# Optimization experiments

Measured on AMD Instinct MI355X. Metric: run time of the kernel, lower is better.

## Reference

```python
import jax, jax.numpy as jnp
import numpy as np

B, T, C, H = 2, 1024, 1024, 16
D = C // H                      # head_dim = 64
NG, BS = 64, 16                 # HBS groups / block_size (1024 = 64*16)
SQ = 32                         # sqrt_dim (1024 = 32*32)


def layer_norm(x, g, b, eps=1e-5):
    m = jnp.mean(x, axis=-1, keepdims=True)
    v = jnp.var(x, axis=-1, keepdims=True)
    return (x - m) * jax.lax.rsqrt(v + eps) * g + b


def hbs_proj(x, pre_g, pre_b, block_w, w_row, w_col, alpha, bias):
    # HierarchicalBlockShuffleLayer forward (dim=1024, no padding needed)
    xn = layer_norm(x, pre_g, pre_b)
    x_flat = xn.reshape(-1, C)
    # block mixing: per-group 16x16 matmul, then flip feature axis
    g = x_flat.reshape(-1, NG, BS)
    y_mixed = jnp.einsum('ngi,gij->ngj', g, block_w).reshape(-1, C)
    block_out = y_mixed[..., ::-1]
    # monarch branch: 32x32 grid, right-multiply W_col then W_row^T
    grid = x_flat.reshape(-1, SQ, SQ)
    z = jnp.einsum('nij,jc->nic', grid, w_col)
    z = jnp.einsum('nic,rc->nir', z, w_row).reshape(-1, C)
    out = block_out + alpha * z + bias
    return out.reshape(x.shape)


def setup_inputs() -> dict:
    key = jax.random.key(0)
    ks = jax.random.split(key, 12)
    inp = {
        'x': jax.random.normal(ks[0], (B, T, C), jnp.float32),
        'c_attn_w': jax.random.normal(ks[1], (3 * C, C), jnp.float32) * (1.0 / np.sqrt(C)),
        'c_attn_b': jnp.zeros((3 * C,), jnp.float32),
        'focus_gate': jnp.float32(0.0),
        'attn_norm_g': jnp.ones((D,), jnp.float32),
        'attn_norm_b': jnp.zeros((D,), jnp.float32),
        'out_norm_g': jnp.ones((C,), jnp.float32),
        'out_norm_b': jnp.zeros((C,), jnp.float32),
        'proj_pre_g': jnp.ones((C,), jnp.float32),
        'proj_pre_b': jnp.zeros((C,), jnp.float32),
        'proj_block_w': jax.random.normal(ks[2], (NG, BS, BS), jnp.float32) * 0.5 / np.sqrt(BS),
        'proj_w_row': jax.random.normal(ks[3], (SQ, SQ), jnp.float32) * 0.1 / np.sqrt(SQ),
        'proj_w_col': jax.random.normal(ks[4], (SQ, SQ), jnp.float32) * 0.1 / np.sqrt(SQ),
        'proj_alpha': jnp.float32(0.0),
        'proj_bias': jnp.zeros((C,), jnp.float32),
    }
    return inp


def reference(x, c_attn_w, c_attn_b, focus_gate, attn_norm_g, attn_norm_b,
              out_norm_g, out_norm_b, proj_pre_g, proj_pre_b, proj_block_w,
              proj_w_row, proj_w_col, proj_alpha, proj_bias):
    scale = 1.0 / np.sqrt(D)
    qkv = x @ c_attn_w.T + c_attn_b                      # [B,T,3C]
    q, k, v = jnp.split(qkv, 3, axis=2)
    # [B,H,T,D]
    q = q.reshape(B, T, H, D).transpose(0, 2, 1, 3)
    k = k.reshape(B, T, H, D).transpose(0, 2, 1, 3)
    v = v.reshape(B, T, H, D).transpose(0, 2, 1, 3)

    # --- causal linear attention branch (fp32) ---
    Qp = jax.nn.elu(q * scale) + 1.0
    Kp = jax.nn.elu(k * scale) + 1.0
    KV = jnp.einsum('bhtd,bhte->bhtde', Kp, v)           # [B,H,T,D,D]
    KV_cum = jnp.cumsum(KV, axis=2)
    K_cum = jnp.cumsum(Kp, axis=2)
    numer = jnp.einsum('bhtd,bhtde->bhte', Qp, KV_cum)
    denom = jnp.einsum('bhtd,bhtd->bht', Qp, K_cum)[..., None]
    y_lin = numer / (denom + 1e-4)                       # [B,H,T,D]
    y_lin = layer_norm(y_lin.transpose(0, 2, 1, 3), attn_norm_g, attn_norm_b)
    y_lin = y_lin.transpose(0, 2, 1, 3)

    # --- standard causal SDPA branch ---
    scores = jnp.einsum('bhqd,bhkd->bhqk', q, k) * scale
    causal = jnp.tril(jnp.ones((T, T), bool))
    scores = jnp.where(causal, scores, -jnp.inf)
    attn = jax.nn.softmax(scores, axis=-1)
    y_sharp = jnp.einsum('bhqk,bhkd->bhqd', attn, v)

    # --- gated combine + output projection ---
    alpha = jax.nn.sigmoid(focus_gate)
    y = alpha * y_sharp + (1.0 - alpha) * y_lin
    y = y.transpose(0, 2, 1, 3).reshape(B, T, C)
    y = layer_norm(y, out_norm_g, out_norm_b)
    return hbs_proj(y, proj_pre_g, proj_pre_b, proj_block_w,
                    proj_w_row, proj_w_col, proj_alpha, proj_bias)
```

## Files before the change

kernel.cpp:

```cpp
#include <hip/hip_runtime.h>
#include <math.h>

constexpr int T_ = 1024;
constexpr int C_ = 1024;
constexpr int H_ = 16;
constexpr int D_ = 64;
#define SCALE 0.125f

typedef unsigned short u16;
typedef __attribute__((ext_vector_type(8))) short short8;
typedef __attribute__((ext_vector_type(4))) float f32x4;

__device__ __forceinline__ float elu1(float x) { return x > 0.f ? x + 1.f : expf(x); }

__device__ __forceinline__ u16 f2bf(float f) {
    union { float f; unsigned u; } c; c.f = f;
    unsigned r = (c.u + 0x7fffu + ((c.u >> 16) & 1u)) >> 16;
    return (u16)r;
}
__device__ __forceinline__ float bf2f(u16 u) {
    union { unsigned u; float f; } c; c.u = (unsigned)u << 16;
    return c.f;
}

#define GLL16(g, l)                                                            \
    __builtin_amdgcn_global_load_lds(                                          \
        (const __attribute__((address_space(1))) void*)(g),                    \
        (__attribute__((address_space(3))) void*)(l), 16, 0, 0)

__global__ __launch_bounds__(256) void k0_cast(
    const float* __restrict__ s, u16* __restrict__ d, int n4)
{
    int i = blockIdx.x * 256 + threadIdx.x;
    if (i < n4) {
        float4 v = reinterpret_cast<const float4*>(s)[i];
        ushort4 o;
        o.x = f2bf(v.x); o.y = f2bf(v.y); o.z = f2bf(v.z); o.w = f2bf(v.w);
        reinterpret_cast<ushort4*>(d)[i] = o;
    }
}

__global__ __launch_bounds__(256) void k1_qkv(
    const u16* __restrict__ xbf, const u16* __restrict__ wbf,
    const float* __restrict__ bias,
    u16* __restrict__ qb, u16* __restrict__ kb, u16* __restrict__ vb)
{
    __shared__ __align__(16) u16 As[128 * 32];
    __shared__ __align__(16) u16 Bs[128 * 32];
    const int tid = threadIdx.x;
    const int wave = tid >> 6, lane = tid & 63;
    const int quad = lane >> 4, l15 = lane & 15;
    const int m0 = blockIdx.y << 7, n0 = blockIdx.x << 7;
    const int wm = (wave >> 1) << 6, wn = (wave & 1) << 6;

    const int rowS = (wave << 5) + (lane >> 2);
    const int seg8 = (lane & 3) << 3;
    const u16* gA1 = xbf + (size_t)(m0 + rowS) * 1024 + seg8;
    const u16* gA2 = gA1 + (size_t)16 * 1024;
    const u16* gB1 = wbf + (size_t)(n0 + rowS) * 1024 + seg8;
    const u16* gB2 = gB1 + (size_t)16 * 1024;
    u16* lA1 = &As[(wave << 5) * 32];
    u16* lA2 = lA1 + 16 * 32;
    u16* lB1 = &Bs[(wave << 5) * 32];
    u16* lB2 = lB1 + 16 * 32;

    f32x4 zero4 = {0.f, 0.f, 0.f, 0.f};
    f32x4 acc[4][4];
#pragma unroll
    for (int i = 0; i < 4; i++)
#pragma unroll
        for (int j = 0; j < 4; j++) acc[i][j] = zero4;

    for (int k0 = 0; k0 < 1024; k0 += 32) {
        GLL16(gA1 + k0, lA1);
        GLL16(gA2 + k0, lA2);
        GLL16(gB1 + k0, lB1);
        GLL16(gB2 + k0, lB2);
        __syncthreads();
        short8 a[4], b[4];
#pragma unroll
        for (int mi = 0; mi < 4; mi++)
            a[mi] = *(const short8*)&As[(wm + mi * 16 + l15) * 32 + (quad << 3)];
#pragma unroll
        for (int ni = 0; ni < 4; ni++)
            b[ni] = *(const short8*)&Bs[(wn + ni * 16 + l15) * 32 + (quad << 3)];
#pragma unroll
        for (int mi = 0; mi < 4; mi++)
#pragma unroll
            for (int ni = 0; ni < 4; ni++)
                acc[mi][ni] = __builtin_amdgcn_mfma_f32_16x16x32_bf16(
                    a[mi], b[ni], acc[mi][ni], 0, 0, 0);
        __syncthreads();
    }
#pragma unroll
    for (int ni = 0; ni < 4; ni++) {
        int n_g = n0 + wn + ni * 16 + l15;
        int which = n_g >> 10;
        int h = (n_g >> 6) & 15;
        int d = n_g & 63;
        u16* dst = (which == 0) ? qb : (which == 1) ? kb : vb;
        float bz = bias[n_g];
#pragma unroll
        for (int mi = 0; mi < 4; mi++) {
#pragma unroll
            for (int reg = 0; reg < 4; reg++) {
                int m = m0 + wm + mi * 16 + (quad << 2) + reg;
                int bi = m >> 10, t = m & 1023;
                dst[((size_t)(bi * 16 + h) << 16) + ((size_t)t << 6) + d] =
                    f2bf(acc[mi][ni][reg] + bz);
            }
        }
    }
}

__global__ __launch_bounds__(256) void k_vt(
    const u16* __restrict__ vb, u16* __restrict__ vtb)
{
    const int t0 = blockIdx.x << 6, bh = blockIdx.y;
    __shared__ __align__(16) u16 Vs[64][72];
    const int tid = threadIdx.x;
#pragma unroll
    for (int u = 0; u < 2; u++) {
        int idx = (tid + (u << 8)) << 3;
        int r = idx >> 6, c = idx & 63;
        *(uint4*)&Vs[r][c] =
            *(const uint4*)&vb[((size_t)bh << 16) + ((size_t)(t0 + r) << 6) + c];
    }
    __syncthreads();
#pragma unroll
    for (int u = 0; u < 2; u++) {
        int idx = (tid + (u << 8)) << 3;
        int dd = idx >> 6, c0 = idx & 63;
        union { u16 s[8]; uint4 v; } tmp;
#pragma unroll
        for (int j = 0; j < 8; j++) tmp.s[j] = Vs[c0 + j][dd];
        *(uint4*)&vtb[((size_t)((bh << 6) + dd) << 10) + t0 + c0] = tmp.v;
    }
}

__global__ __launch_bounds__(256) void k2a_chunkkv(
    const u16* __restrict__ kb, const u16* __restrict__ vb,
    float* __restrict__ Sg, float* __restrict__ svg)
{
    const int chunk = blockIdx.x, bh = blockIdx.y;
    const int t0 = chunk << 6;
    __shared__ float Ks[64][65];
    __shared__ float Vs[64][65];
    const int tid = threadIdx.x;
    const u16* kp = kb + (size_t)bh * T_ * D_;
    const u16* vp = vb + (size_t)bh * T_ * D_;
#pragma unroll
    for (int ii = 0; ii < 16; ii++) {
        int idx = tid + (ii << 8);
        int row = idx >> 6, col = idx & 63;
        Ks[row][col] = elu1(bf2f(kp[(size_t)(t0 + row) * D_ + col]) * SCALE);
        Vs[row][col] = bf2f(vp[(size_t)(t0 + row) * D_ + col]);
    }
    __syncthreads();
    const int tr = tid >> 4, tc = tid & 15;
    const int d0 = tr * 4, e0 = tc * 4;
    float acc[4][4] = {};
    for (int c = 0; c < 64; c++) {
        float a[4], b[4];
#pragma unroll
        for (int i = 0; i < 4; i++) a[i] = Ks[c][d0 + i];
#pragma unroll
        for (int j = 0; j < 4; j++) b[j] = Vs[c][e0 + j];
#pragma unroll
        for (int i = 0; i < 4; i++)
#pragma unroll
            for (int j = 0; j < 4; j++) acc[i][j] += a[i] * b[j];
    }
    float* so = Sg + ((size_t)bh * 16 + chunk) * 4096;
#pragma unroll
    for (int i = 0; i < 4; i++) {
        float4 o = {acc[i][0], acc[i][1], acc[i][2], acc[i][3]};
        *reinterpret_cast<float4*>(&so[(d0 + i) * 64 + e0]) = o;
    }
    if (tc == 0) {
#pragma unroll
        for (int i = 0; i < 4; i++) {
            float s = 0.f;
            for (int c = 0; c < 64; c++) s += Ks[c][d0 + i];
            svg[((size_t)bh * 16 + chunk) * 64 + d0 + i] = s;
        }
    }
}

__global__ __launch_bounds__(256) void k2s_scan(
    float* __restrict__ Sg, float* __restrict__ svg)
{
    int gid = blockIdx.x * 256 + threadIdx.x;
    if (gid < 131072) {
        int bh = gid >> 12, e = gid & 4095;
        float* base = Sg + ((size_t)bh << 16) + e;
        float v[16];
#pragma unroll
        for (int c = 0; c < 16; c++) v[c] = base[(size_t)c << 12];
        float run = 0.f;
#pragma unroll
        for (int c = 0; c < 16; c++) {
            base[(size_t)c << 12] = run;
            run += v[c];
        }
    } else if (gid < 131072 + 2048) {
        int g2 = gid - 131072;
        int bh = g2 >> 6, d = g2 & 63;
        float* base = svg + ((size_t)bh << 10) + d;
        float v[16];
#pragma unroll
        for (int c = 0; c < 16; c++) v[c] = base[c << 6];
        float run = 0.f;
#pragma unroll
        for (int c = 0; c < 16; c++) {
            base[c << 6] = run;
            run += v[c];
        }
    }
}

__global__ __launch_bounds__(256) void k2b_lin(
    const u16* __restrict__ qbp, const u16* __restrict__ kbp,
    const u16* __restrict__ vbp,
    const float* __restrict__ Sg, const float* __restrict__ svg,
    const float* __restrict__ ang, const float* __restrict__ anb,
    float* __restrict__ ylin)
{
    const int chunk = blockIdx.x, bh = blockIdx.y;
    const int t0 = chunk << 6;
    __shared__ __align__(16) float bufA[64][68];
    __shared__ float bufQ[64][65];
    __shared__ float bufK[64][65];
    __shared__ float svec[64];
    const int tid = threadIdx.x;
    const u16* qp = qbp + (size_t)bh * T_ * D_;
    const u16* kp = kbp + (size_t)bh * T_ * D_;
    const u16* vp = vbp + (size_t)bh * T_ * D_;
    const float* sp = Sg + (((size_t)bh * 16 + chunk) << 12);
#pragma unroll
    for (int u = 0; u < 4; u++) {
        int idx = (tid + (u << 8)) << 2;
        int dd = idx >> 6, e = idx & 63;
        *(float4*)&bufA[dd][e] = *(const float4*)&sp[idx];
    }
    if (tid < 64) svec[tid] = svg[(((size_t)bh * 16 + chunk) << 6) + tid];
#pragma unroll
    for (int ii = 0; ii < 16; ii++) {
        int idx = tid + (ii << 8);
        int row = idx >> 6, col = idx & 63;
        bufQ[col][row] = elu1(bf2f(qp[(size_t)(t0 + row) * D_ + col]) * SCALE);
    }
    __syncthreads();
    const int tr = tid >> 4, tc = tid & 15;
    const int r0 = tr * 4, c0 = tc * 4;
    float N[4][4] = {};
    float pden[4];
    for (int dd = 0; dd < 64; dd++) {
        float a[4], b[4];
#pragma unroll
        for (int i = 0; i < 4; i++) a[i] = bufQ[dd][r0 + i];
#pragma unroll
        for (int j = 0; j < 4; j++) b[j] = bufA[dd][c0 + j];
#pragma unroll
        for (int i = 0; i < 4; i++)
#pragma unroll
            for (int j = 0; j < 4; j++) N[i][j] += a[i] * b[j];
    }
#pragma unroll
    for (int i = 0; i < 4; i++) {
        float s = 0.f;
#pragma unroll
        for (int j = 0; j < 4; j++) s += bufQ[c0 + j][r0 + i] * svec[c0 + j];
        pden[i] = s;
    }
    __syncthreads();
#pragma unroll
    for (int ii = 0; ii < 16; ii++) {
        int idx = tid + (ii << 8);
        int row = idx >> 6, col = idx & 63;
        bufK[col][row] = elu1(bf2f(kp[(size_t)(t0 + row) * D_ + col]) * SCALE);
        bufA[row][col] = bf2f(vp[(size_t)(t0 + row) * D_ + col]);
    }
    __syncthreads();
    float sc[4][4] = {};
    for (int dd = 0; dd < 64; dd++) {
        float a[4], b[4];
#pragma unroll
        for (int i = 0; i < 4; i++) a[i] = bufQ[dd][r0 + i];
#pragma unroll
        for (int j = 0; j < 4; j++) b[j] = bufK[dd][c0 + j];
#pragma unroll
        for (int i = 0; i < 4; i++)
#pragma unroll
            for (int j = 0; j < 4; j++) sc[i][j] += a[i] * b[j];
    }
    __syncthreads();
#pragma unroll
    for (int i = 0; i < 4; i++) {
        float s = 0.f;
#pragma unroll
        for (int j = 0; j < 4; j++) {
            float pv = ((c0 + j) <= (r0 + i)) ? sc[i][j] : 0.f;
            bufQ[c0 + j][r0 + i] = pv;
            s += pv;
        }
        pden[i] += s;
    }
#pragma unroll
    for (int i = 0; i < 4; i++) {
#pragma unroll
        for (int off = 1; off < 16; off <<= 1)
            pden[i] += __shfl_xor(pden[i], off);
    }
    __syncthreads();
    for (int c = 0; c < 64; c++) {
        float a[4], b[4];
#pragma unroll
        for (int i = 0; i < 4; i++) a[i] = bufQ[c][r0 + i];
#pragma unroll
        for (int j = 0; j < 4; j++) b[j] = bufA[c][c0 + j];
#pragma unroll
        for (int i = 0; i < 4; i++)
#pragma unroll
            for (int j = 0; j < 4; j++) N[i][j] += a[i] * b[j];
    }
    float yv[4][4], s1[4], s2[4];
#pragma unroll
    for (int i = 0; i < 4; i++) {
        float inv = 1.f / (pden[i] + 1e-4f);
        s1[i] = 0.f; s2[i] = 0.f;
#pragma unroll
        for (int j = 0; j < 4; j++) {
            float t = N[i][j] * inv;
            yv[i][j] = t; s1[i] += t; s2[i] += t * t;
        }
    }
#pragma unroll
    for (int i = 0; i < 4; i++) {
#pragma unroll
        for (int off = 1; off < 16; off <<= 1) {
            s1[i] += __shfl_xor(s1[i], off);
            s2[i] += __shfl_xor(s2[i], off);
        }
    }
#pragma unroll
    for (int i = 0; i < 4; i++) {
        float mean = s1[i] * (1.f / 64.f);
        float var = s2[i] * (1.f / 64.f) - mean * mean;
        float rstd = rsqrtf(var + 1e-5f);
        float4 o;
        o.x = (yv[i][0] - mean) * rstd * ang[c0 + 0] + anb[c0 + 0];
        o.y = (yv[i][1] - mean) * rstd * ang[c0 + 1] + anb[c0 + 1];
        o.z = (yv[i][2] - mean) * rstd * ang[c0 + 2] + anb[c0 + 2];
        o.w = (yv[i][3] - mean) * rstd * ang[c0 + 3] + anb[c0 + 3];
        *reinterpret_cast<float4*>(
            &ylin[((size_t)bh * T_ + t0 + r0 + i) * D_ + c0]) = o;
    }
}

__global__ __launch_bounds__(256) void k3_sharp(
    const u16* __restrict__ qbp, const u16* __restrict__ kbp,
    const u16* __restrict__ vtb,
    const float* __restrict__ ylin, const float* __restrict__ fg,
    float* __restrict__ ycomb)
{
    const int bh = blockIdx.y;
    __shared__ __align__(16) u16 Qs[64][72];
    __shared__ __align__(16) u16 Ks[64][72];
    __shared__ __align__(16) u16 Vt[64][72];
    __shared__ __align__(16) u16 Pa[64][72];
    const int tid = threadIdx.x;
    const int wave = tid >> 6, lane = tid & 63;
    const int quad = lane >> 4, l15 = lane & 15;
    const float al = 1.f / (1.f + expf(-fg[0]));
    const int bi = bh >> 4, h = bh & 15;
    const f32x4 zero4 = {0.f, 0.f, 0.f, 0.f};

    for (int phase = 0; phase < 2; phase++) {
        const int qi = phase == 0 ? (int)blockIdx.x : 15 - (int)blockIdx.x;
        __syncthreads();
#pragma unroll
        for (int u = 0; u < 2; u++) {
            int idx = (tid + (u << 8)) << 3;
            int r = idx >> 6, c = idx & 63;
            *(uint4*)&Qs[r][c] = *(const uint4*)
                &qbp[((size_t)bh << 16) + ((size_t)((qi << 6) + r) << 6) + c];
        }
        __syncthreads();
        short8 bq[2];
        bq[0] = *(const short8*)&Qs[(wave << 4) + l15][(quad << 3)];
        bq[1] = *(const short8*)&Qs[(wave << 4) + l15][32 + (quad << 3)];
        f32x4 O[4];
#pragma unroll
        for (int dt = 0; dt < 4; dt++) O[dt] = zero4;
        float m_run = -INFINITY, l_run = 0.f;
        const int r_g = (qi << 6) + (wave << 4) + l15;

        for (int ki = 0; ki <= qi; ki++) {
            __syncthreads();
#pragma unroll
            for (int u = 0; u < 2; u++) {
                int idx = (tid + (u << 8)) << 3;
                int r = idx >> 6, c = idx & 63;
                *(uint4*)&Ks[r][c] = *(const uint4*)
                    &kbp[((size_t)bh << 16) + ((size_t)((ki << 6) + r) << 6) + c];
                *(uint4*)&Vt[r][c] = *(const uint4*)
                    &vtb[((size_t)((bh << 6) + r) << 10) + (ki << 6) + c];
            }
            __syncthreads();
            f32x4 st[4];
#pragma unroll
            for (int ct = 0; ct < 4; ct++) st[ct] = zero4;
#pragma unroll
            for (int ks = 0; ks < 2; ks++) {
#pragma unroll
                for (int ct = 0; ct < 4; ct++) {
                    short8 a = *(const short8*)
                        &Ks[(ct << 4) + l15][(ks << 5) + (quad << 3)];
                    st[ct] = __builtin_amdgcn_mfma_f32_16x16x32_bf16(
                        a, bq[ks], st[ct], 0, 0, 0);
                }
            }
            float mloc = -INFINITY;
#pragma unroll
            for (int ct = 0; ct < 4; ct++)
#pragma unroll
                for (int reg = 0; reg < 4; reg++) {
                    int c_g = (ki << 6) + (ct << 4) + (quad << 2) + reg;
                    float s = st[ct][reg] * SCALE;
                    if (c_g > r_g) s = -INFINITY;
                    st[ct][reg] = s;
                    mloc = fmaxf(mloc, s);
                }
            mloc = fmaxf(mloc, __shfl_xor(mloc, 16));
            mloc = fmaxf(mloc, __shfl_xor(mloc, 32));
            float mnew = fmaxf(m_run, mloc);
            float corr = __expf(m_run - mnew);
            m_run = mnew;
            float rsum = 0.f;
#pragma unroll
            for (int ct = 0; ct < 4; ct++) {
                u16 pk[4];
#pragma unroll
                for (int reg = 0; reg < 4; reg++) {
                    float pv = __expf(st[ct][reg] - mnew);
                    rsum += pv;
                    pk[reg] = f2bf(pv);
                }
                unsigned lo = (unsigned)pk[0] | ((unsigned)pk[1] << 16);
                unsigned hi = (unsigned)pk[2] | ((unsigned)pk[3] << 16);
                uint2 pkv; pkv.x = lo; pkv.y = hi;
                *(uint2*)&Pa[(wave << 4) + l15][(ct << 4) + (quad << 2)] = pkv;
            }
            rsum += __shfl_xor(rsum, 16);
            rsum += __shfl_xor(rsum, 32);
            l_run = l_run * corr + rsum;
            float co[4];
#pragma unroll
            for (int reg = 0; reg < 4; reg++)
                co[reg] = __shfl(corr, ((lane >> 4) << 2) + reg);
#pragma unroll
            for (int dt = 0; dt < 4; dt++)
#pragma unroll
                for (int reg = 0; reg < 4; reg++) O[dt][reg] *= co[reg];
#pragma unroll
            for (int ks = 0; ks < 2; ks++) {
                short8 ap = *(const short8*)
                    &Pa[(wave << 4) + l15][(ks << 5) + (quad << 3)];
#pragma unroll
                for (int dt = 0; dt < 4; dt++) {
                    short8 bv = *(const short8*)
                        &Vt[(dt << 4) + l15][(ks << 5) + (quad << 3)];
                    O[dt] = __builtin_amdgcn_mfma_f32_16x16x32_bf16(
                        ap, bv, O[dt], 0, 0, 0);
                }
            }
        }
        float lo4[4];
#pragma unroll
        for (int reg = 0; reg < 4; reg++)
            lo4[reg] = __shfl(l_run, ((lane >> 4) << 2) + reg);
#pragma unroll
        for (int reg = 0; reg < 4; reg++) {
            int t = (qi << 6) + (wave << 4) + (quad << 2) + reg;
            float inv = al / lo4[reg];
#pragma unroll
            for (int dt = 0; dt < 4; dt++) {
                int d = (dt << 4) + l15;
                float yl = ylin[(((size_t)bh << 10) + t) * 64 + d];
                ycomb[((size_t)((bi << 10) + t) << 10) + (h << 6) + d] =
                    O[dt][reg] * inv + (1.f - al) * yl;
            }
        }
    }
}

__global__ __launch_bounds__(256) void k4m(
    const float* __restrict__ wcol, const float* __restrict__ wrow,
    const float* __restrict__ palpha, float* __restrict__ Mg)
{
    const int tid = threadIdx.x;
    const int j = tid >> 3, r0 = (tid & 7) << 2;
    const float al = palpha[0];
    float acc[4] = {0.f, 0.f, 0.f, 0.f};
    for (int c = 0; c < 32; c++) {
        float wc = wcol[(j << 5) + c];
#pragma unroll
        for (int q = 0; q < 4; q++) acc[q] += wc * wrow[((r0 + q) << 5) + c];
    }
    float4 o = {al * acc[0], al * acc[1], al * acc[2], al * acc[3]};
    *reinterpret_cast<float4*>(&Mg[(j << 5) + r0]) = o;
}

__global__ __launch_bounds__(256) void k4_proj(
    const float* __restrict__ ycomb,
    const float* __restrict__ og, const float* __restrict__ ob,
    const float* __restrict__ pg, const float* __restrict__ pb,
    const float* __restrict__ bw, const float* __restrict__ Mg,
    const float* __restrict__ pbias, float* __restrict__ out)
{
    const int tok = blockIdx.x;
    __shared__ float xb[1024];
    __shared__ float red[8];
    const int tid = threadIdx.x;
    const int c0 = tid << 2;
    const float* yrow = ycomb + ((size_t)tok << 10);
    float4 v4 = *reinterpret_cast<const float4*>(yrow + c0);
    float v[4] = {v4.x, v4.y, v4.z, v4.w};
    float s1 = v[0] + v[1] + v[2] + v[3];
    float s2 = v[0]*v[0] + v[1]*v[1] + v[2]*v[2] + v[3]*v[3];
#pragma unroll
    for (int off = 1; off < 64; off <<= 1) {
        s1 += __shfl_xor(s1, off); s2 += __shfl_xor(s2, off);
    }
    if ((tid & 63) == 0) { red[(tid >> 6) * 2] = s1; red[(tid >> 6) * 2 + 1] = s2; }
    __syncthreads();
    s1 = red[0] + red[2] + red[4] + red[6];
    s2 = red[1] + red[3] + red[5] + red[7];
    __syncthreads();
    {
        float mean = s1 * (1.f / 1024.f);
        float var = s2 * (1.f / 1024.f) - mean * mean;
        float rstd = rsqrtf(var + 1e-5f);
#pragma unroll
        for (int q = 0; q < 4; q++)
            v[q] = (v[q] - mean) * rstd * og[c0 + q] + ob[c0 + q];
    }
    s1 = v[0] + v[1] + v[2] + v[3];
    s2 = v[0]*v[0] + v[1]*v[1] + v[2]*v[2] + v[3]*v[3];
#pragma unroll
    for (int off = 1; off < 64; off <<= 1) {
        s1 += __shfl_xor(s1, off); s2 += __shfl_xor(s2, off);
    }
    if ((tid & 63) == 0) { red[(tid >> 6) * 2] = s1; red[(tid >> 6) * 2 + 1] = s2; }
    __syncthreads();
    s1 = red[0] + red[2] + red[4] + red[6];
    s2 = red[1] + red[3] + red[5] + red[7];
    {
        float mean = s1 * (1.f / 1024.f);
        float var = s2 * (1.f / 1024.f) - mean * mean;
        float rstd = rsqrtf(var + 1e-5f);
#pragma unroll
        for (int q = 0; q < 4; q++)
            xb[c0 + q] = (v[q] - mean) * rstd * pg[c0 + q] + pb[c0 + q];
    }
    __syncthreads();
    const int g = tid >> 2;
    const int jb = (tid & 3) << 2;
    float acc[4] = {0.f, 0.f, 0.f, 0.f};
    {
        const float* xg = &xb[g << 4];
        const float* bwg = &bw[(g << 8) + jb];
        for (int i = 0; i < 16; i++) {
            float xv = xg[i];
            float4 wv = *reinterpret_cast<const float4*>(&bwg[i << 4]);
            acc[0] += xv * wv.x; acc[1] += xv * wv.y;
            acc[2] += xv * wv.z; acc[3] += xv * wv.w;
        }
    }
    const int C0 = ((63 - g) << 4) + 12 - jb;
    const int i2 = C0 >> 5, r0 = C0 & 31;
    float z2[4] = {0.f, 0.f, 0.f, 0.f};
    {
        const float* xg = &xb[i2 << 5];
        const float* mg = &Mg[r0];
        for (int j = 0; j < 32; j++) {
            float xv = xg[j];
            float4 mv = *reinterpret_cast<const float4*>(&mg[j << 5]);
            z2[0] += xv * mv.x; z2[1] += xv * mv.y;
            z2[2] += xv * mv.z; z2[3] += xv * mv.w;
        }
    }
    float4 bz = *reinterpret_cast<const float4*>(&pbias[C0]);
    float4 o;
    o.x = acc[3] + z2[0] + bz.x;
    o.y = acc[2] + z2[1] + bz.y;
    o.z = acc[1] + z2[2] + bz.z;
    o.w = acc[0] + z2[3] + bz.w;
    *reinterpret_cast<float4*>(&out[((size_t)tok << 10) + C0]) = o;
}

extern "C" void kernel_launch(void* const* d_in, const int* in_sizes, int n_in,
                              void* d_out, int out_size, void* d_ws, size_t ws_size,
                              hipStream_t stream) {
    const float* x   = (const float*)d_in[0];
    const float* w   = (const float*)d_in[1];
    const float* wb  = (const float*)d_in[2];
    const float* fg  = (const float*)d_in[3];
    const float* ang = (const float*)d_in[4];
    const float* anb = (const float*)d_in[5];
    const float* ong = (const float*)d_in[6];
    const float* onb = (const float*)d_in[7];
    const float* ppg = (const float*)d_in[8];
    const float* ppb = (const float*)d_in[9];
    const float* pbw = (const float*)d_in[10];
    const float* pwr = (const float*)d_in[11];
    const float* pwc = (const float*)d_in[12];
    const float* pal = (const float*)d_in[13];
    const float* pbi = (const float*)d_in[14];

    uint8_t* p = (uint8_t*)d_ws;
    u16* xbf = (u16*)p;  p += (size_t)2048 * 1024 * 2;
    u16* wbf = (u16*)p;  p += (size_t)3072 * 1024 * 2;
    u16* qb  = (u16*)p;  p += (size_t)32 * 1024 * 64 * 2;
    u16* kb  = (u16*)p;  p += (size_t)32 * 1024 * 64 * 2;
    u16* vb  = (u16*)p;  p += (size_t)32 * 1024 * 64 * 2;
    u16* vtb = (u16*)p;  p += (size_t)32 * 1024 * 64 * 2;
    float* ylin  = (float*)p;  p += (size_t)32 * 1024 * 64 * 4;
    float* ycomb = (float*)p;  p += (size_t)32 * 1024 * 64 * 4;
    float* Sg    = (float*)p;  p += (size_t)32 * 16 * 4096 * 4;
    float* svg   = (float*)p;  p += (size_t)32 * 16 * 64 * 4;
    float* Mg    = (float*)p;  p += (size_t)32 * 32 * 4;
    float* out   = (float*)d_out;

    k0_cast<<<2048, 256, 0, stream>>>(x, xbf, 524288);
    k0_cast<<<3072, 256, 0, stream>>>(w, wbf, 786432);
    k4m<<<1, 256, 0, stream>>>(pwc, pwr, pal, Mg);
    k1_qkv<<<dim3(24, 16), 256, 0, stream>>>(xbf, wbf, wb, qb, kb, vb);
    k_vt<<<dim3(16, 32), 256, 0, stream>>>(vb, vtb);
    k2a_chunkkv<<<dim3(16, 32), 256, 0, stream>>>(kb, vb, Sg, svg);
    k2s_scan<<<521, 256, 0, stream>>>(Sg, svg);
    k2b_lin<<<dim3(16, 32), 256, 0, stream>>>(qb, kb, vb, Sg, svg, ang, anb, ylin);
    k3_sharp<<<dim3(8, 32), 256, 0, stream>>>(qb, kb, vtb, ylin, fg, ycomb);
    k4_proj<<<2048, 256, 0, stream>>>(ycomb, ong, onb, ppg, ppb, pbw, Mg, pbi, out);
}
```

Baseline: 225.5 us.

## Split causal attention KV range into two partial blocks and merge in separate kernel

```diff
diff --git a/kernel.cpp b/kernel.cpp
--- a/kernel.cpp
+++ b/kernel.cpp
@@ -358,13 +358,17 @@
     }
 }
 
-__global__ __launch_bounds__(256) void k3_sharp(
+__global__ __launch_bounds__(256) void k3a_part(
     const u16* __restrict__ qbp, const u16* __restrict__ kbp,
     const u16* __restrict__ vtb,
-    const float* __restrict__ ylin, const float* __restrict__ fg,
-    float* __restrict__ ycomb)
-{
-    const int bh = blockIdx.y;
+    float* __restrict__ Op, float* __restrict__ ml)
+{
+    const int job = blockIdx.x, bh = blockIdx.y;
+    const int qi = job >> 1, half = job & 1;
+    const int n = qi + 1;
+    const int csplit = n >> 1;
+    const int kbeg = half ? csplit : 0;
+    const int kend = half ? n : csplit;
     __shared__ __align__(16) u16 Qs[64][72];
     __shared__ __align__(16) u16 Ks[64][72];
     __shared__ __align__(16) u16 Vt[64][72];
@@ -372,126 +376,162 @@
     const int tid = threadIdx.x;
     const int wave = tid >> 6, lane = tid & 63;
     const int quad = lane >> 4, l15 = lane & 15;
-    const float al = 1.f / (1.f + expf(-fg[0]));
-    const int bi = bh >> 4, h = bh & 15;
     const f32x4 zero4 = {0.f, 0.f, 0.f, 0.f};
 
-    for (int phase = 0; phase < 2; phase++) {
-        const int qi = phase == 0 ? (int)blockIdx.x : 15 - (int)blockIdx.x;
+#pragma unroll
+    for (int u = 0; u < 2; u++) {
+        int idx = (tid + (u << 8)) << 3;
+        int r = idx >> 6, c = idx & 63;
+        *(uint4*)&Qs[r][c] = *(const uint4*)
+            &qbp[((size_t)bh << 16) + ((size_t)((qi << 6) + r) << 6) + c];
+    }
+    __syncthreads();
+    short8 bq[2];
+    bq[0] = *(const short8*)&Qs[(wave << 4) + l15][(quad << 3)];
+    bq[1] = *(const short8*)&Qs[(wave << 4) + l15][32 + (quad << 3)];
+    f32x4 O[4];
+#pragma unroll
+    for (int dt = 0; dt < 4; dt++) O[dt] = zero4;
+    float m_run = -INFINITY, l_run = 0.f;
+    const int r_g = (qi << 6) + (wave << 4) + l15;
+
+    for (int ki = kbeg; ki < kend; ki++) {
         __syncthreads();
 #pragma unroll
         for (int u = 0; u < 2; u++) {
             int idx = (tid + (u << 8)) << 3;
             int r = idx >> 6, c = idx & 63;
-            *(uint4*)&Qs[r][c] = *(const uint4*)
-                &qbp[((size_t)bh << 16) + ((size_t)((qi << 6) + r) << 6) + c];
+            *(uint4*)&Ks[r][c] = *(const uint4*)
+                &kbp[((size_t)bh << 16) + ((size_t)((ki << 6) + r) << 6) + c];
+            *(uint4*)&Vt[r][c] = *(const uint4*)
+                &vtb[((size_t)((bh << 6) + r) << 10) + (ki << 6) + c];
         }
         __syncthreads();
-        short8 bq[2];
-        bq[0] = *(const short8*)&Qs[(wave << 4) + l15][(quad << 3)];
-        bq[1] = *(const short8*)&Qs[(wave << 4) + l15][32 + (quad << 3)];
-        f32x4 O[4];
-#pragma unroll
-        for (int dt = 0; dt < 4; dt++) O[dt] = zero4;
-        float m_run = -INFINITY, l_run = 0.f;
-        const int r_g = (qi << 6) + (wave << 4) + l15;
-
-        for (int ki = 0; ki <= qi; ki++) {
-            __syncthreads();
-#pragma unroll
-            for (int u = 0; u < 2; u++) {
-                int idx = (tid + (u << 8)) << 3;
-                int r = idx >> 6, c = idx & 63;
-                *(uint4*)&Ks[r][c] = *(const uint4*)
-                    &kbp[((size_t)bh << 16) + ((size_t)((ki << 6) + r) << 6) + c];
-                *(uint4*)&Vt[r][c] = *(const uint4*)
-                    &vtb[((size_t)((bh << 6) + r) << 10) + (ki << 6) + c];
+        f32x4 st[4];
+#pragma unroll
+        for (int ct = 0; ct < 4; ct++) st[ct] = zero4;
+#pragma unroll
+        for (int ks = 0; ks < 2; ks++) {
+#pragma unroll
+            for (int ct = 0; ct < 4; ct++) {
+                short8 a = *(const short8*)
+                    &Ks[(ct << 4) + l15][(ks << 5) + (quad << 3)];
+                st[ct] = __builtin_amdgcn_mfma_f32_16x16x32_bf16(
+                    a, bq[ks], st[ct], 0, 0, 0);
             }
-            __syncthreads();
-            f32x4 st[4];
-#pragma unroll
-            for (int ct = 0; ct < 4; ct++) st[ct] = zero4;
-#pragma unroll
-            for (int ks = 0; ks < 2; ks++) {
-#pragma unroll
-                for (int ct = 0; ct < 4; ct++) {
-                    short8 a = *(const short8*)
-                        &Ks[(ct << 4) + l15][(ks << 5) + (quad << 3)];
-                    st[ct] = __builtin_amdgcn_mfma_f32_16x16x32_bf16(
-                        a, bq[ks], st[ct], 0, 0, 0);
-                }
+        }
+        float mloc = -INFINITY;
+#pragma unroll
+        for (int ct = 0; ct < 4; ct++)
+#pragma unroll
+            for (int reg = 0; reg < 4; reg++) {
+                int c_g = (ki << 6) + (ct << 4) + (quad << 2) + reg;
+                float s = st[ct][reg] * SCALE;
+                if (c_g > r_g) s = -INFINITY;
+                st[ct][reg] = s;
+                mloc = fmaxf(mloc, s);
             }
-            float mloc = -INFINITY;
-#pragma unroll
-            for (int ct = 0; ct < 4; ct++)
-#pragma unroll
-                for (int reg = 0; reg < 4; reg++) {
-                    int c_g = (ki << 6) + (ct << 4) + (quad << 2) + reg;
-                    float s = st[ct][reg] * SCALE;
-                    if (c_g > r_g) s = -INFINITY;
-                    st[ct][reg] = s;
-                    mloc = fmaxf(mloc, s);
-                }
-            mloc = fmaxf(mloc, __shfl_xor(mloc, 16));
-            mloc = fmaxf(mloc, __shfl_xor(mloc, 32));
-            float mnew = fmaxf(m_run, mloc);
-            float corr = __expf(m_run - mnew);
-            m_run = mnew;
-            float rsum = 0.f;
-#pragma unroll
-            for (int ct = 0; ct < 4; ct++) {
-                u16 pk[4];
-#pragma unroll
-                for (int reg = 0; reg < 4; reg++) {
-                    float pv = __expf(st[ct][reg] - mnew);
-                    rsum += pv;
-                    pk[reg] = f2bf(pv);
-                }
-                unsigned lo = (unsigned)pk[0] | ((unsigned)pk[1] << 16);
-                unsigned hi = (unsigned)pk[2] | ((unsigned)pk[3] << 16);
-                uint2 pkv; pkv.x = lo; pkv.y = hi;
-                *(uint2*)&Pa[(wave << 4) + l15][(ct << 4) + (quad << 2)] = pkv;
+        mloc = fmaxf(mloc, __shfl_xor(mloc, 16));
+        mloc = fmaxf(mloc, __shfl_xor(mloc, 32));
+        float mnew = fmaxf(m_run, mloc);
+        float corr = __expf(m_run - mnew);
+        m_run = mnew;
+        float rsum = 0.f;
+#pragma unroll
+        for (int ct = 0; ct < 4; ct++) {
+            u16 pk[4];
+#pragma unroll
+            for (int reg = 0; reg < 4; reg++) {
+                float pv = __expf(st[ct][reg] - mnew);
+                rsum += pv;
+                pk[reg] = f2bf(pv);
             }
-            rsum += __shfl_xor(rsum, 16);
-            rsum += __shfl_xor(rsum, 32);
-            l_run = l_run * corr + rsum;
-            float co[4];
-#pragma unroll
-            for (int reg = 0; reg < 4; reg++)
-                co[reg] = __shfl(corr, ((lane >> 4) << 2) + reg);
-#pragma unroll
-            for (int dt = 0; dt < 4; dt++)
-#pragma unroll
-                for (int reg = 0; reg < 4; reg++) O[dt][reg] *= co[reg];
-#pragma unroll
-            for (int ks = 0; ks < 2; ks++) {
-                short8 ap = *(const short8*)
-                    &Pa[(wave << 4) + l15][(ks << 5) + (quad << 3)];
-#pragma unroll
-                for (int dt = 0; dt < 4; dt++) {
-                    short8 bv = *(const short8*)
-                        &Vt[(dt << 4) + l15][(ks << 5) + (quad << 3)];
-                    O[dt] = __builtin_amdgcn_mfma_f32_16x16x32_bf16(
-                        ap, bv, O[dt], 0, 0, 0);
-                }
+            unsigned lo = (unsigned)pk[0] | ((unsigned)pk[1] << 16);
+            unsigned hi = (unsigned)pk[2] | ((unsigned)pk[3] << 16);
+            uint2 pkv; pkv.x = lo; pkv.y = hi;
+            *(uint2*)&Pa[(wave << 4) + l15][(ct << 4) + (quad << 2)] = pkv;
+        }
+        rsum += __shfl_xor(rsum, 16);
+        rsum += __shfl_xor(rsum, 32);
+        l_run = l_run * corr + rsum;
+        float co[4];
+#pragma unroll
+        for (int reg = 0; reg < 4; reg++)
+            co[reg] = __shfl(corr, ((lane >> 4) << 2) + reg);
+#pragma unroll
+        for (int dt = 0; dt < 4; dt++)
+#pragma unroll
+            for (int reg = 0; reg < 4; reg++) O[dt][reg] *= co[reg];
+#pragma unroll
+        for (int ks = 0; ks < 2; ks++) {
+            short8 ap = *(const short8*)
+                &Pa[(wave << 4) + l15][(ks << 5) + (quad << 3)];
+#pragma unroll
+            for (int dt = 0; dt < 4; dt++) {
+                short8 bv = *(const short8*)
+                    &Vt[(dt << 4) + l15][(ks << 5) + (quad << 3)];
+                O[dt] = __builtin_amdgcn_mfma_f32_16x16x32_bf16(
+                    ap, bv, O[dt], 0, 0, 0);
             }
         }
-        float lo4[4];
-#pragma unroll
-        for (int reg = 0; reg < 4; reg++)
-            lo4[reg] = __shfl(l_run, ((lane >> 4) << 2) + reg);
+    }
+    float* ob = Op + (((size_t)bh * 32 + job) << 12);
+#pragma unroll
+    for (int dt = 0; dt < 4; dt++)
 #pragma unroll
         for (int reg = 0; reg < 4; reg++) {
-            int t = (qi << 6) + (wave << 4) + (quad << 2) + reg;
-            float inv = al / lo4[reg];
-#pragma unroll
-            for (int dt = 0; dt < 4; dt++) {
-                int d = (dt << 4) + l15;
-                float yl = ylin[(((size_t)bh << 10) + t) * 64 + d];
-                ycomb[((size_t)((bi << 10) + t) << 10) + (h << 6) + d] =
-                    O[dt][reg] * inv + (1.f - al) * yl;
-            }
-        }
+            int r = (wave << 4) + (quad << 2) + reg;
+            int d = (dt << 4) + l15;
+            ob[(r << 6) + d] = O[dt][reg];
+        }
+    if (quad == 0) {
+        int r = (wave << 4) + l15;
+        float* mlb = ml + (((size_t)bh * 32 + job) << 7);
+        mlb[r] = m_run;
+        mlb[64 + r] = l_run;
+    }
+}
+
+__global__ __launch_bounds__(256) void k3c_comb(
+    const float* __restrict__ Op, const float* __restrict__ ml,
+    const float* __restrict__ ylin, const float* __restrict__ fg,
+    float* __restrict__ ycomb)
+{
+    const int qi = blockIdx.x, bh = blockIdx.y;
+    const int bi = bh >> 4, h = bh & 15;
+    __shared__ float sm[4][64];
+    const int tid = threadIdx.x;
+    const float al = 1.f / (1.f + __expf(-fg[0]));
+    const size_t b0 = (((size_t)bh * 32 + (qi << 1)) << 7);
+    if (tid < 64) {
+        sm[0][tid] = ml[b0 + tid];
+        sm[1][tid] = ml[b0 + 64 + tid];
+        sm[2][tid] = ml[b0 + 128 + tid];
+        sm[3][tid] = ml[b0 + 192 + tid];
+    }
+    __syncthreads();
+    const float* o0 = Op + (((size_t)bh * 32 + (qi << 1)) << 12);
+    const float* o1 = o0 + 4096;
+#pragma unroll
+    for (int u = 0; u < 4; u++) {
+        int idx = tid + (u << 8);
+        int r = idx >> 4, d4 = (idx & 15) << 2;
+        float m0 = sm[0][r], l0 = sm[1][r];
+        float m1 = sm[2][r], l1 = sm[3][r];
+        float m = fmaxf(m0, m1);
+        float w0 = (m0 == -INFINITY) ? 0.f : __expf(m0 - m);
+        float w1 = __expf(m1 - m);
+        float inv = al / (l0 * w0 + l1 * w1);
+        float4 a = *(const float4*)&o0[(r << 6) + d4];
+        float4 b = *(const float4*)&o1[(r << 6) + d4];
+        int t = (qi << 6) + r;
+        float4 yl = *(const float4*)&ylin[((((size_t)bh << 10) + t) << 6) + d4];
+        float4 o;
+        o.x = (a.x * w0 + b.x * w1) * inv + (1.f - al) * yl.x;
+        o.y = (a.y * w0 + b.y * w1) * inv + (1.f - al) * yl.y;
+        o.z = (a.z * w0 + b.z * w1) * inv + (1.f - al) * yl.z;
+        o.w = (a.w * w0 + b.w * w1) * inv + (1.f - al) * yl.w;
+        *(float4*)&ycomb[((((size_t)(bi << 10) + t)) << 10) + (h << 6) + d4] = o;
     }
 }
 
@@ -631,6 +671,8 @@
     float* Sg    = (float*)p;  p += (size_t)32 * 16 * 4096 * 4;
     float* svg   = (float*)p;  p += (size_t)32 * 16 * 64 * 4;
     float* Mg    = (float*)p;  p += (size_t)32 * 32 * 4;
+    float* Op    = (float*)p;  p += (size_t)32 * 32 * 4096 * 4;
+    float* ml    = (float*)p;  p += (size_t)32 * 32 * 128 * 4;
     float* out   = (float*)d_out;
 
     k0_cast<<<2048, 256, 0, stream>>>(x, xbf, 524288);
@@ -641,6 +683,7 @@
     k2a_chunkkv<<<dim3(16, 32), 256, 0, stream>>>(kb, vb, Sg, svg);
     k2s_scan<<<521, 256, 0, stream>>>(Sg, svg);
     k2b_lin<<<dim3(16, 32), 256, 0, stream>>>(qb, kb, vb, Sg, svg, ang, anb, ylin);
-    k3_sharp<<<dim3(8, 32), 256, 0, stream>>>(qb, kb, vtb, ylin, fg, ycomb);
+    k3a_part<<<dim3(32, 32), 256, 0, stream>>>(qb, kb, vtb, Op, ml);
+    k3c_comb<<<dim3(16, 32), 256, 0, stream>>>(Op, ml, ylin, fg, ycomb);
     k4_proj<<<2048, 256, 0, stream>>>(ycomb, ong, onb, ppg, ppb, pbw, Mg, pbi, out);
 }
```

Measured after the change: 216.4 us. -4.0%, faster.
